# Optimization experiments

Measured on AMD Instinct MI355X. Metric: run time of the kernel, lower is better.

Reference implementation:

```python
import jax, jax.numpy as jnp
import numpy as np

H = 12  # num_heads

def _attn(q, k, v):
    # q,k,v: [B,H,N,D]; SDPA default scale 1/sqrt(D)
    D = q.shape[-1]
    scores = jnp.einsum('bhnd,bhmd->bhnm', q, k) / jnp.sqrt(jnp.asarray(D, q.dtype))
    p = jax.nn.softmax(scores, axis=-1)
    return jnp.einsum('bhnm,bhmd->bhnd', p, v)

def setup_inputs() -> dict:
    key = jax.random.key(0)
    ks = jax.random.split(key, 5)
    B, N, C = 2, 2048, 768
    s = 0.02
    return {
        'x': jax.random.normal(ks[0], (B, N, C), jnp.float32),
        'Wq': jax.random.normal(ks[1], (C, 2 * C), jnp.float32) * s,
        'Wk': jax.random.normal(ks[2], (C, 2 * C), jnp.float32) * s,
        'Wv': jax.random.normal(ks[3], (C, C), jnp.float32) * s,
        'lambda_p': jnp.zeros((H, 1, 1), jnp.float32),
        'Wo': jax.random.normal(ks[4], (C, C), jnp.float32) * s,
        'bo': jnp.zeros((C,), jnp.float32),
    }

def reference(x, Wq, Wk, Wv, lambda_p, Wo, bo):
    B, N, C = x.shape
    D = C // H
    # [B,N,2C] -> [2,B,H,N,D]
    q = (x @ Wq).reshape(B, N, 2, H, D).transpose(2, 0, 3, 1, 4)
    k = (x @ Wk).reshape(B, N, 2, H, D).transpose(2, 0, 3, 1, 4)
    v = (x @ Wv).reshape(B, N, H, D).transpose(0, 2, 1, 3)
    out1 = _attn(q[0], k[0], v)
    out2 = _attn(q[1], k[1], v)
    lam = jnp.exp(lambda_p)  # [H,1,1] broadcasts over [B,H,N,D]
    out = out1 - lam * out2
    out = out.transpose(0, 2, 1, 3).reshape(B, N, C)
    return out @ Wo + bo
```

## Files before the change

### kernel.cpp

```cpp
#include <hip/hip_runtime.h>

typedef unsigned short u16;
typedef unsigned int u32;
typedef unsigned long long u64;
typedef __bf16 bf16x8 __attribute__((ext_vector_type(8)));
typedef float f32x4 __attribute__((ext_vector_type(4)));
typedef float f32x16 __attribute__((ext_vector_type(16)));

#define B_ 2
#define N_ 2048
#define C_ 768
#define H_ 12
#define M_ 4096
#define SCALE_LOG2 0.18033688011112042f

#define KSTR 136
#define PSTR 72
#define K1OFF 8704
#define VOFF 17408
#define POFF 26112
#define PWSZ 2304
#define SMSZ 35328

static __device__ __forceinline__ u16 f2bf(float f) {
  u32 u = __builtin_bit_cast(u32, f);
  u32 r = u + 0x7fffu + ((u >> 16) & 1u);
  return (u16)(r >> 16);
}
static __device__ __forceinline__ float fexp2(float x) {
#if __has_builtin(__builtin_amdgcn_exp2f)
  return __builtin_amdgcn_exp2f(x);
#else
  return __expf(x * 0.6931471805599453f);
#endif
}
static __device__ __forceinline__ u32 pack_bf16(float a, float b) {
  u32 r;
  asm("v_cvt_pk_bf16_f32 %0, %1, %2" : "=v"(r) : "v"(a), "v"(b));
  return r;
}
static __device__ __forceinline__ bf16x8 mk8(uint2 a, uint2 b) {
  uint4 u = make_uint4(a.x, a.y, b.x, b.y);
  return __builtin_bit_cast(bf16x8, u);
}

static __device__ __forceinline__ void gload16(const void* g, void* lds_base) {
  __builtin_amdgcn_global_load_lds(
      (__attribute__((address_space(1))) void*)(u64)(g),
      (__attribute__((address_space(3))) void*)(u32)(u64)(lds_base), 16, 0, 0);
}

__global__ __launch_bounds__(256) void k_prep(const float* __restrict__ x,
                                              const float* __restrict__ Wq,
                                              const float* __restrict__ Wk,
                                              const float* __restrict__ Wv,
                                              const float* __restrict__ Wo,
                                              u16* __restrict__ xb,
                                              u16* __restrict__ wqkt,
                                              u16* __restrict__ wvo) {
  const int id = blockIdx.x;
  const int t = threadIdx.x;
  if (id < 3072) {
    int i = id * 256 + t;
    float4 v = ((const float4*)x)[i];
    ushort4 o;
    o.x = f2bf(v.x); o.y = f2bf(v.y); o.z = f2bf(v.z); o.w = f2bf(v.w);
    ((ushort4*)xb)[i] = o;
    return;
  }
  __shared__ float tt[32][33];
  const float* W;
  u16* dst;
  int bx, by;
  if (id < 5376) {
    int rem = id - 3072;
    int z = rem / 1152, r2 = rem % 1152;
    bx = r2 % 48; by = r2 / 48;
    W = z ? Wk : Wq;
    dst = wqkt + (u64)z * 1536 * 768;
    const int N = 1536;
    int n0 = bx * 32, k0 = by * 32;
    int tx = t & 31, ty = t >> 5;
#pragma unroll
    for (int i = 0; i < 4; i++)
      tt[ty + i * 8][tx] = W[(u64)(k0 + ty + i * 8) * N + n0 + tx];
    __syncthreads();
#pragma unroll
    for (int i = 0; i < 4; i++)
      dst[(u64)(n0 + ty + i * 8) * 768 + k0 + tx] = f2bf(tt[tx][ty + i * 8]);
  } else {
    int rem = id - 5376;
    int z = rem / 576, r3 = rem % 576;
    bx = r3 % 24; by = r3 / 24;
    W = z ? Wo : Wv;
    dst = wvo + (u64)z * 768 * 768;
    const int N = 768;
    int n0 = bx * 32, k0 = by * 32;
    int tx = t & 31, ty = t >> 5;
#pragma unroll
    for (int i = 0; i < 4; i++)
      tt[ty + i * 8][tx] = W[(u64)(k0 + ty + i * 8) * N + n0 + tx];
    __syncthreads();
#pragma unroll
    for (int i = 0; i < 4; i++)
      dst[(u64)(n0 + ty + i * 8) * 768 + k0 + tx] = f2bf(tt[tx][ty + i * 8]);
  }
}

__global__ __launch_bounds__(256) void k_gemm_qkv(const u16* __restrict__ A,
                                                  const u16* __restrict__ WQK,
                                                  const u16* __restrict__ WV,
                                                  u16* __restrict__ QKb,
                                                  u16* __restrict__ Vtout) {
  __shared__ u16 As[128 * 32];
  __shared__ u16 Bs[128 * 32];
  const int t = threadIdx.x;
  const int w = t >> 6, l = t & 63;
  const int wr = w >> 1, wc = w & 1;
  const int la = l & 15, lg = l >> 4;
  const int srow = l >> 2, scb = (l & 3) << 4;
  const int by = blockIdx.y;
  const bool isV = by >= 24;

  f32x4 acc[4][4];
#pragma unroll
  for (int i = 0; i < 4; i++)
#pragma unroll
    for (int j = 0; j < 4; j++) acc[i][j] = f32x4{0.f, 0.f, 0.f, 0.f};

  const u16* Ag = A + (u64)(blockIdx.x * 128) * 768;
  const u16* Bg = isV ? WV + (u64)((by - 24) * 128) * 768 : WQK + (u64)(by * 128) * 768;

  for (int k0 = 0; k0 < 768; k0 += 32) {
#pragma unroll
    for (int j = 0; j < 2; j++) {
      int r = (w * 2 + j) * 16 + srow;
      gload16((const char*)(Ag + (u64)r * 768 + k0) + scb, (char*)As + (w * 2 + j) * 1024);
      gload16((const char*)(Bg + (u64)r * 768 + k0) + scb, (char*)Bs + (w * 2 + j) * 1024);
    }
    __syncthreads();
    bf16x8 af[4], bfr[4];
#pragma unroll
    for (int m = 0; m < 4; m++)
      af[m] = *(const bf16x8*)(As + (wr * 64 + m * 16 + la) * 32 + lg * 8);
#pragma unroll
    for (int n = 0; n < 4; n++)
      bfr[n] = *(const bf16x8*)(Bs + (wc * 64 + n * 16 + la) * 32 + lg * 8);
#pragma unroll
    for (int m = 0; m < 4; m++)
#pragma unroll
      for (int n = 0; n < 4; n++)
        acc[m][n] =
            __builtin_amdgcn_mfma_f32_16x16x32_bf16(af[m], bfr[n], acc[m][n], 0, 0, 0);
    __syncthreads();
  }

#pragma unroll
  for (int m = 0; m < 4; m++) {
#pragma unroll
    for (int n = 0; n < 4; n++) {
      int grow0 = blockIdx.x * 128 + wr * 64 + m * 16 + lg * 4;
      if (!isV) {
        int gcol = by * 128 + wc * 64 + n * 16 + la;
        float sc = (gcol < 1536) ? SCALE_LOG2 : 1.0f;
#pragma unroll
        for (int j = 0; j < 4; j++)
          QKb[(u64)(grow0 + j) * 3072 + gcol] = f2bf(acc[m][n][j] * sc);
      } else {
        int gcol = (by - 24) * 128 + wc * 64 + n * 16 + la;
        ushort4 o;
        o.x = f2bf(acc[m][n][0]); o.y = f2bf(acc[m][n][1]);
        o.z = f2bf(acc[m][n][2]); o.w = f2bf(acc[m][n][3]);
        *(ushort4*)(Vtout + (u64)gcol * M_ + grow0) = o;
      }
    }
  }
}

__global__ __launch_bounds__(256) void k_gemm_out(const u16* __restrict__ A,
                                                  const u16* __restrict__ Bt,
                                                  float* __restrict__ Cout,
                                                  const float* __restrict__ bias) {
  __shared__ u16 As[128 * 32];
  __shared__ u16 Bs[128 * 32];
  const int t = threadIdx.x;
  const int w = t >> 6, l = t & 63;
  const int wr = w >> 1, wc = w & 1;
  const int la = l & 15, lg = l >> 4;
  const int srow = l >> 2, scb = (l & 3) << 4;

  f32x4 acc[4][4];
#pragma unroll
  for (int i = 0; i < 4; i++)
#pragma unroll
    for (int j = 0; j < 4; j++) acc[i][j] = f32x4{0.f, 0.f, 0.f, 0.f};

  const u16* Ag = A + (u64)(blockIdx.x * 128) * 768;
  const u16* Bg = Bt + (u64)(blockIdx.y * 128) * 768;

  for (int k0 = 0; k0 < 768; k0 += 32) {
#pragma unroll
    for (int j = 0; j < 2; j++) {
      int r = (w * 2 + j) * 16 + srow;
      gload16((const char*)(Ag + (u64)r * 768 + k0) + scb, (char*)As + (w * 2 + j) * 1024);
      gload16((const char*)(Bg + (u64)r * 768 + k0) + scb, (char*)Bs + (w * 2 + j) * 1024);
    }
    __syncthreads();
    bf16x8 af[4], bfr[4];
#pragma unroll
    for (int m = 0; m < 4; m++)
      af[m] = *(const bf16x8*)(As + (wr * 64 + m * 16 + la) * 32 + lg * 8);
#pragma unroll
    for (int n = 0; n < 4; n++)
      bfr[n] = *(const bf16x8*)(Bs + (wc * 64 + n * 16 + la) * 32 + lg * 8);
#pragma unroll
    for (int m = 0; m < 4; m++)
#pragma unroll
      for (int n = 0; n < 4; n++)
        acc[m][n] =
            __builtin_amdgcn_mfma_f32_16x16x32_bf16(af[m], bfr[n], acc[m][n], 0, 0, 0);
    __syncthreads();
  }

#pragma unroll
  for (int m = 0; m < 4; m++) {
#pragma unroll
    for (int n = 0; n < 4; n++) {
      int grow0 = blockIdx.x * 128 + wr * 64 + m * 16 + lg * 4;
      int gcol = blockIdx.y * 128 + wc * 64 + n * 16 + la;
      float bb = bias[gcol];
#pragma unroll
      for (int j = 0; j < 4; j++)
        Cout[(u64)(grow0 + j) * 768 + gcol] = acc[m][n][j] + bb;
    }
  }
}

__global__ __launch_bounds__(256, 2) void k_attn7(const u16* __restrict__ QKb,
                                                  const u16* __restrict__ Vt,
                                                  const float* __restrict__ lamp,
                                                  u16* __restrict__ Ob) {
  const int hw = blockIdx.x;
  const int wid = (hw & 7) * 96 + (hw >> 3);
  const int qt = wid & 31;
  const int hb = wid >> 5;
  const int h = hb % H_, b = hb / H_;

  __shared__ __align__(16) char smem[SMSZ];
  const int t = threadIdx.x, w = t >> 6, l = t & 63;
  const int p = w >> 1, kvh = w & 1;
  const int ql = l & 31, hh = l >> 5;

  bf16x8 qf[2][4];
#pragma unroll
  for (int s = 0; s < 2; s++) {
    const u16* qrow =
        QKb + (u64)(b * N_ + qt * 64 + s * 32 + ql) * 3072 + p * 768 + h * 64 + hh * 8;
#pragma unroll
    for (int c = 0; c < 4; c++) qf[s][c] = *(const bf16x8*)(qrow + 16 * c);
  }

  f32x16 oacc[2][2];
#pragma unroll
  for (int s = 0; s < 2; s++)
#pragma unroll
    for (int dh = 0; dh < 2; dh++)
#pragma unroll
      for (int r = 0; r < 16; r++) oacc[s][dh][r] = 0.f;
  float l_run[2] = {0.f, 0.f};

  const int rA = t >> 3, cb = (t & 7) << 4;
  const char* kg = (const char*)(QKb + (u64)(b * N_ + rA) * 3072 + 1536 + h * 64) + cb;
  const char* vg = (const char*)(Vt + (u64)(h * 64 + rA) * M_ + b * N_) + cb;
  const u64 KR32 = (u64)32 * 3072 * 2;
  const u64 VR32 = (u64)32 * M_ * 2;
  const u64 KSTEP = (u64)64 * 3072 * 2;
  char* d0a = smem + rA * KSTR + cb;
  char* d0b = smem + (rA + 32) * KSTR + cb;

  uint4 rk0A, rk0B, rk1A, rk1B, rvA, rvB;
#define LOADS6()                              \
  do {                                        \
    rk0A = *(const uint4*)(kg);               \
    rk0B = *(const uint4*)(kg + KR32);        \
    rk1A = *(const uint4*)(kg + 1536);        \
    rk1B = *(const uint4*)(kg + 1536 + KR32); \
    rvA = *(const uint4*)(vg);                \
    rvB = *(const uint4*)(vg + VR32);         \
  } while (0)
  LOADS6();

  const char* kbase = smem + p * K1OFF + (32 * kvh + ql) * KSTR + 16 * hh;
  const char* vb0 = smem + VOFF + ql * KSTR + 64 * kvh + 16 * hh;
  const char* vb1 = smem + VOFF + (32 + ql) * KSTR + 64 * kvh + 16 * hh;
  char* pb = smem + POFF + w * PWSZ;
  char* pwr = pb + ql * PSTR + 8 * hh;
  const char* prd = pb + ql * PSTR + 16 * hh;

  for (int kt = 0; kt < 32; kt++) {
    asm volatile("s_waitcnt vmcnt(0)" ::: "memory");
    __builtin_amdgcn_sched_barrier(0);
    *(uint2*)(d0a) = make_uint2(rk0A.x, rk0A.y);
    *(uint2*)(d0a + 8) = make_uint2(rk0A.z, rk0A.w);
    *(uint2*)(d0b) = make_uint2(rk0B.x, rk0B.y);
    *(uint2*)(d0b + 8) = make_uint2(rk0B.z, rk0B.w);
    *(uint2*)(d0a + K1OFF) = make_uint2(rk1A.x, rk1A.y);
    *(uint2*)(d0a + K1OFF + 8) = make_uint2(rk1A.z, rk1A.w);
    *(uint2*)(d0b + K1OFF) = make_uint2(rk1B.x, rk1B.y);
    *(uint2*)(d0b + K1OFF + 8) = make_uint2(rk1B.z, rk1B.w);
    *(uint2*)(d0a + VOFF) = make_uint2(rvA.x, rvA.y);
    *(uint2*)(d0a + VOFF + 8) = make_uint2(rvA.z, rvA.w);
    *(uint2*)(d0b + VOFF) = make_uint2(rvB.x, rvB.y);
    *(uint2*)(d0b + VOFF + 8) = make_uint2(rvB.z, rvB.w);
    asm volatile("s_waitcnt lgkmcnt(0)" ::: "memory");
    __builtin_amdgcn_s_barrier();
    kg += KSTEP;
    vg += 128;
    if (kt < 31) LOADS6();
    __builtin_amdgcn_sched_barrier(0);

    bf16x8 kf[4];
#pragma unroll
    for (int c = 0; c < 4; c++)
      kf[c] = mk8(*(const uint2*)(kbase + 32 * c), *(const uint2*)(kbase + 32 * c + 8));
    bf16x8 vf[2][2];
#pragma unroll
    for (int dh = 0; dh < 2; dh++) {
      const char* vb = dh ? vb1 : vb0;
#pragma unroll
      for (int c2 = 0; c2 < 2; c2++)
        vf[dh][c2] =
            mk8(*(const uint2*)(vb + 32 * c2), *(const uint2*)(vb + 32 * c2 + 8));
    }

#pragma unroll
    for (int s = 0; s < 2; s++) {
      f32x16 st;
#pragma unroll
      for (int r = 0; r < 16; r++) st[r] = 0.f;
      __builtin_amdgcn_s_setprio(1);
#pragma unroll
      for (int c = 0; c < 4; c++)
        st = __builtin_amdgcn_mfma_f32_32x32x16_bf16(kf[c], qf[s][c], st, 0, 0, 0);
      __builtin_amdgcn_s_setprio(0);

      float sm[16];
#pragma unroll
      for (int r = 0; r < 16; r++) {
        st[r] = fexp2(st[r]);
        sm[r] = st[r];
      }
#pragma unroll
      for (int sd = 8; sd >= 1; sd >>= 1)
#pragma unroll
        for (int r = 0; r < sd; r++) sm[r] += sm[r + sd];
      l_run[s] += sm[0] + __shfl_xor(sm[0], 32, 64);

#pragma unroll
      for (int g = 0; g < 4; g++) {
        uint2 pk;
        pk.x = pack_bf16(st[4 * g + 0], st[4 * g + 1]);
        pk.y = pack_bf16(st[4 * g + 2], st[4 * g + 3]);
        *(uint2*)(pwr + 16 * g) = pk;
      }
      bf16x8 pa[2];
#pragma unroll
      for (int c2 = 0; c2 < 2; c2++)
        pa[c2] =
            mk8(*(const uint2*)(prd + 32 * c2), *(const uint2*)(prd + 32 * c2 + 8));

      __builtin_amdgcn_s_setprio(1);
#pragma unroll
      for (int c2 = 0; c2 < 2; c2++)
#pragma unroll
        for (int dh = 0; dh < 2; dh++)
          oacc[s][dh] = __builtin_amdgcn_mfma_f32_32x32x16_bf16(pa[c2], vf[dh][c2],
                                                                oacc[s][dh], 0, 0, 0);
      __builtin_amdgcn_s_setprio(0);
    }
    __builtin_amdgcn_s_barrier();
  }

  float* Os = (float*)smem;
  float* lsc = (float*)(smem + 32768);
  __syncthreads();
  if (kvh == 1) {
#pragma unroll
    for (int s = 0; s < 2; s++) {
#pragma unroll
      for (int dh = 0; dh < 2; dh++)
#pragma unroll
        for (int r = 0; r < 16; r++) {
          int q = s * 32 + (r & 3) + 8 * (r >> 2) + 4 * hh;
          Os[(p * 64 + q) * 64 + dh * 32 + ql] = oacc[s][dh][r];
        }
      lsc[p * 64 + s * 32 + ql] = l_run[s];
    }
  }
  __syncthreads();
  if (kvh == 0) {
#pragma unroll
    for (int s = 0; s < 2; s++) {
#pragma unroll
      for (int dh = 0; dh < 2; dh++)
#pragma unroll
        for (int r = 0; r < 16; r++) {
          int q = s * 32 + (r & 3) + 8 * (r >> 2) + 4 * hh;
          oacc[s][dh][r] += Os[(p * 64 + q) * 64 + dh * 32 + ql];
        }
      l_run[s] += lsc[p * 64 + s * 32 + ql];
    }
  }
  __syncthreads();
  if (kvh == 0 && p == 1) {
    float lam = __expf(lamp[h]);
    float inv[2] = {lam / l_run[0], lam / l_run[1]};
#pragma unroll
    for (int s = 0; s < 2; s++)
#pragma unroll
      for (int dh = 0; dh < 2; dh++)
#pragma unroll
        for (int r = 0; r < 16; r++) {
          int qm = (r & 3) + 8 * (r >> 2) + 4 * hh;
          float iT = __shfl(inv[s], qm, 64);
          Os[(64 + s * 32 + qm) * 64 + dh * 32 + ql] = oacc[s][dh][r] * iT;
        }
  }
  __syncthreads();
  if (kvh == 0 && p == 0) {
    float inv[2] = {1.f / l_run[0], 1.f / l_run[1]};
    u16* Og = Ob + (u64)(b * N_ + qt * 64) * C_ + h * 64;
#pragma unroll
    for (int s = 0; s < 2; s++)
#pragma unroll
      for (int dh = 0; dh < 2; dh++)
#pragma unroll
        for (int r = 0; r < 16; r++) {
          int qm = (r & 3) + 8 * (r >> 2) + 4 * hh;
          float iT = __shfl(inv[s], qm, 64);
          int q = s * 32 + qm, d = dh * 32 + ql;
          float v = oacc[s][dh][r] * iT - Os[(64 + q) * 64 + d];
          Og[(u64)q * C_ + d] = f2bf(v);
        }
  }
}

extern "C" void kernel_launch(void* const* d_in, const int* in_sizes, int n_in,
                              void* d_out, int out_size, void* d_ws, size_t ws_size,
                              hipStream_t stream) {
  const float* x = (const float*)d_in[0];
  const float* Wq = (const float*)d_in[1];
  const float* Wk = (const float*)d_in[2];
  const float* Wv = (const float*)d_in[3];
  const float* lamp = (const float*)d_in[4];
  const float* Wo = (const float*)d_in[5];
  const float* bo = (const float*)d_in[6];

  char* ws = (char*)d_ws;
  u16* xb = (u16*)ws;    ws += (u64)M_ * C_ * 2;
  u16* wqkt = (u16*)ws;  ws += (u64)4 * C_ * C_ * 2;
  u16* wvo = (u16*)ws;   ws += (u64)2 * C_ * C_ * 2;
  u16* QKb = (u16*)ws;   ws += (u64)M_ * 4 * C_ * 2;
  u16* Vt = (u16*)ws;    ws += (u64)C_ * M_ * 2;
  u16* Ob = (u16*)ws;    ws += (u64)M_ * C_ * 2;
  u16* wvt = wvo;
  u16* wot = wvo + (u64)C_ * C_;

  k_prep<<<dim3(6528), 256, 0, stream>>>(x, Wq, Wk, Wv, Wo, xb, wqkt, wvo);
  k_gemm_qkv<<<dim3(32, 30), 256, 0, stream>>>(xb, wqkt, wvt, QKb, Vt);
  k_attn7<<<dim3(768), 256, 0, stream>>>(QKb, Vt, lamp, Ob);
  k_gemm_out<<<dim3(32, 6), 256, 0, stream>>>(Ob, wot, (float*)d_out, bo);
}
```

Before: 145.7 us.

## Overlap shared-memory staging of next K/V tile with attention compute

The attention loop now loads the current K/V fragments from shared memory into registers and then synchronizes. It immediately writes the next tile, already prefetched into registers, into shared memory and issues the global loads for the tile after that, all before running the MFMA and softmax work. This hides the global-load wait and the LDS write latency behind compute, instead of stalling at the start of every iteration. In exchange it adds a second full block barrier per iteration and keeps more data in flight in registers, which may add register pressure.

```diff
diff --git a/kernel.cpp b/kernel.cpp
--- a/kernel.cpp
+++ b/kernel.cpp
@@ -236,10 +236,10 @@
   }
 }
 
-__global__ __launch_bounds__(256, 2) void k_attn7(const u16* __restrict__ QKb,
-                                                  const u16* __restrict__ Vt,
-                                                  const float* __restrict__ lamp,
-                                                  u16* __restrict__ Ob) {
+__global__ __launch_bounds__(256, 2) void k_attn13(const u16* __restrict__ QKb,
+                                                   const u16* __restrict__ Vt,
+                                                   const float* __restrict__ lamp,
+                                                   u16* __restrict__ Ob) {
   const int hw = blockIdx.x;
   const int wid = (hw & 7) * 96 + (hw >> 3);
   const int qt = wid & 31;
@@ -288,7 +288,21 @@
     rvA = *(const uint4*)(vg);                \
     rvB = *(const uint4*)(vg + VR32);         \
   } while (0)
-  LOADS6();
+#define STAGE()                                              \
+  do {                                                       \
+    *(uint2*)(d0a) = make_uint2(rk0A.x, rk0A.y);             \
+    *(uint2*)(d0a + 8) = make_uint2(rk0A.z, rk0A.w);         \
+    *(uint2*)(d0b) = make_uint2(rk0B.x, rk0B.y);             \
+    *(uint2*)(d0b + 8) = make_uint2(rk0B.z, rk0B.w);         \
+    *(uint2*)(d0a + K1OFF) = make_uint2(rk1A.x, rk1A.y);     \
+    *(uint2*)(d0a + K1OFF + 8) = make_uint2(rk1A.z, rk1A.w); \
+    *(uint2*)(d0b + K1OFF) = make_uint2(rk1B.x, rk1B.y);     \
+    *(uint2*)(d0b + K1OFF + 8) = make_uint2(rk1B.z, rk1B.w); \
+    *(uint2*)(d0a + VOFF) = make_uint2(rvA.x, rvA.y);        \
+    *(uint2*)(d0a + VOFF + 8) = make_uint2(rvA.z, rvA.w);    \
+    *(uint2*)(d0b + VOFF) = make_uint2(rvB.x, rvB.y);        \
+    *(uint2*)(d0b + VOFF + 8) = make_uint2(rvB.z, rvB.w);    \
+  } while (0)
 
   const char* kbase = smem + p * K1OFF + (32 * kvh + ql) * KSTR + 16 * hh;
   const char* vb0 = smem + VOFF + ql * KSTR + 64 * kvh + 16 * hh;
@@ -297,28 +311,14 @@
   char* pwr = pb + ql * PSTR + 8 * hh;
   const char* prd = pb + ql * PSTR + 16 * hh;
 
+  LOADS6();
+  STAGE();
+  kg += KSTEP;
+  vg += 128;
+  LOADS6();
+  __syncthreads();
+
   for (int kt = 0; kt < 32; kt++) {
-    asm volatile("s_waitcnt vmcnt(0)" ::: "memory");
-    __builtin_amdgcn_sched_barrier(0);
-    *(uint2*)(d0a) = make_uint2(rk0A.x, rk0A.y);
-    *(uint2*)(d0a + 8) = make_uint2(rk0A.z, rk0A.w);
-    *(uint2*)(d0b) = make_uint2(rk0B.x, rk0B.y);
-    *(uint2*)(d0b + 8) = make_uint2(rk0B.z, rk0B.w);
-    *(uint2*)(d0a + K1OFF) = make_uint2(rk1A.x, rk1A.y);
-    *(uint2*)(d0a + K1OFF + 8) = make_uint2(rk1A.z, rk1A.w);
-    *(uint2*)(d0b + K1OFF) = make_uint2(rk1B.x, rk1B.y);
-    *(uint2*)(d0b + K1OFF + 8) = make_uint2(rk1B.z, rk1B.w);
-    *(uint2*)(d0a + VOFF) = make_uint2(rvA.x, rvA.y);
-    *(uint2*)(d0a + VOFF + 8) = make_uint2(rvA.z, rvA.w);
-    *(uint2*)(d0b + VOFF) = make_uint2(rvB.x, rvB.y);
-    *(uint2*)(d0b + VOFF + 8) = make_uint2(rvB.z, rvB.w);
-    asm volatile("s_waitcnt lgkmcnt(0)" ::: "memory");
-    __builtin_amdgcn_s_barrier();
-    kg += KSTEP;
-    vg += 128;
-    if (kt < 31) LOADS6();
-    __builtin_amdgcn_sched_barrier(0);
-
     bf16x8 kf[4];
 #pragma unroll
     for (int c = 0; c < 4; c++)
@@ -331,6 +331,14 @@
       for (int c2 = 0; c2 < 2; c2++)
         vf[dh][c2] =
             mk8(*(const uint2*)(vb + 32 * c2), *(const uint2*)(vb + 32 * c2 + 8));
+    }
+    __syncthreads();
+
+    if (kt < 31) {
+      STAGE();
+      kg += KSTEP;
+      vg += 128;
+      if (kt < 30) LOADS6();
     }
 
 #pragma unroll
@@ -378,7 +386,7 @@
                                                                 oacc[s][dh], 0, 0, 0);
       __builtin_amdgcn_s_setprio(0);
     }
-    __builtin_amdgcn_s_barrier();
+    __syncthreads();
   }
 
   float* Os = (float*)smem;
@@ -468,6 +476,6 @@
 
   k_prep<<<dim3(6528), 256, 0, stream>>>(x, Wq, Wk, Wv, Wo, xb, wqkt, wvo);
   k_gemm_qkv<<<dim3(32, 30), 256, 0, stream>>>(xb, wqkt, wvt, QKb, Vt);
-  k_attn7<<<dim3(768), 256, 0, stream>>>(QKb, Vt, lamp, Ob);
+  k_attn13<<<dim3(768), 256, 0, stream>>>(QKb, Vt, lamp, Ob);
   k_gemm_out<<<dim3(32, 6), 256, 0, stream>>>(Ob, wot, (float*)d_out, bo);
 }
```

After: 146.2 us. No clear change (+0.4%).
